# Optimization experiments

Hardware: AMD Instinct MI355X
Metric: run time of the kernel (lower is better)

## Reference

```python
import jax, jax.numpy as jnp
import numpy as np

BATCH = 2048
INPUT_SIZE = 2048
OUTPUT_SIZE = 2048
N_INPUTS = 6            # fan-in per LUT node
K = 1 << N_INPUTS       # 64 table entries per node


def setup_inputs() -> dict:
    key = jax.random.key(0)
    k1, k2, k3 = jax.random.split(key, 3)
    x = jax.random.uniform(k1, (BATCH, INPUT_SIZE), dtype=jnp.float32)
    table = jax.random.normal(k2, (OUTPUT_SIZE, K), dtype=jnp.float32)
    mapping = jax.random.randint(k3, (OUTPUT_SIZE, N_INPUTS), 0, INPUT_SIZE, dtype=jnp.int64)
    return {"x": x, "table": table, "mapping": mapping}


def reference(x, table, mapping):
    # x: (B, I) in [0,1]; table: (O, 2^n) raw logits; mapping: (O, n) int indices
    O, n = mapping.shape
    Kv = 1 << n
    # per-node input gather -> (B, O, n)
    xg = x[:, mapping]
    # binary codes of the 2^n LUT vertices: bits[k, i] = i-th bit of k
    bits = ((jnp.arange(Kv)[:, None] >> jnp.arange(n)[None, :]) & 1).astype(x.dtype)  # (K, n)
    # vertex probabilities prod_i (x_i if bit else 1-x_i), built by a tiny fixed loop over n
    probs = jnp.ones((x.shape[0], O, Kv), dtype=x.dtype)
    for i in range(n):
        xi = xg[:, :, i][:, :, None]                      # (B, O, 1)
        bi = bits[:, i][None, None, :]                    # (1, 1, K)
        probs = probs * (xi * bi + (1.0 - xi) * (1.0 - bi))
    # differentiable LUT lookup: expected table value under vertex distribution
    out = jnp.einsum('bok,ok->bo', probs, jax.nn.sigmoid(table))  # (B, O)
    return out
```

## Files before the change

### kernel.cpp

```cpp
#include <hip/hip_runtime.h>
#include <math.h>

#define B_TOTAL 2048
#define I_TOTAL 2048
#define O_TOTAL 2048
#define KW 64
#define NIN 6
#define BLOCK 256

#define WS_SIGW 0
#define WS_M32  (512 * 1024)
#define WS_XT   (1024 * 1024)
#define WS_OUTT (WS_XT + B_TOTAL * I_TOTAL * 4)

__global__ void prep_kernel(const float* __restrict__ table,
                            const unsigned int* __restrict__ map_raw,
                            float* __restrict__ sigw,
                            int* __restrict__ m32)
{
    int idx = blockIdx.x * blockDim.x + threadIdx.x;
    int k = idx & 63;
    float s = 1.0f / (1.0f + __expf(-table[idx]));
    float v = s;
    if (k >= 32) {
        float s0 = 1.0f / (1.0f + __expf(-table[idx - 32]));
        v = s - s0;
    }
    sigw[idx] = v;

    if (idx < O_TOTAL * NIN) {
        bool is64 = ((map_raw[1] | map_raw[3] | map_raw[5] | map_raw[7]) == 0u);
        m32[idx] = is64 ? (int)map_raw[2 * idx] : (int)map_raw[idx];
    }
}

__global__ __launch_bounds__(256) void transpose_k(const float* __restrict__ src,
                                                   float* __restrict__ dst)
{
    __shared__ float tile[64][65];
    const int t  = threadIdx.x;
    const int r0 = blockIdx.y * 64;
    const int c0 = blockIdx.x * 64;
    const int rr = t >> 4;
    const int cc = (t & 15) << 2;
    #pragma unroll
    for (int p = 0; p < 4; ++p) {
        int r = p * 16 + rr;
        float4 v = *(const float4*)(src + (size_t)(r0 + r) * 2048 + c0 + cc);
        tile[r][cc + 0] = v.x; tile[r][cc + 1] = v.y;
        tile[r][cc + 2] = v.z; tile[r][cc + 3] = v.w;
    }
    __syncthreads();
    #pragma unroll
    for (int p = 0; p < 4; ++p) {
        int r = p * 16 + rr;
        float4 v;
        v.x = tile[cc + 0][r]; v.y = tile[cc + 1][r];
        v.z = tile[cc + 2][r]; v.w = tile[cc + 3][r];
        *(float4*)(dst + (size_t)(c0 + r) * 2048 + r0 + cc) = v;
    }
}

__global__ __launch_bounds__(BLOCK) void lut_main(
    const float* __restrict__ xT,
    const float* __restrict__ sigw,
    const int*   __restrict__ m32,
    float*       __restrict__ outT)
{
    const int wave = threadIdx.x >> 6;
    const int lane = threadIdx.x & 63;
    const int o    = blockIdx.y * 4 + wave;
    const int b0   = blockIdx.x * 512;

    float ww[KW];
    const float* wp = sigw + (size_t)o * KW;
    #pragma unroll
    for (int k = 0; k < KW; ++k) ww[k] = wp[k];

    int m[NIN];
    #pragma unroll
    for (int i = 0; i < NIN; ++i) m[i] = m32[o * NIN + i];

    #pragma unroll
    for (int p = 0; p < 8; ++p) {
        const int b = b0 + p * 64 + lane;
        float xv[NIN];
        #pragma unroll
        for (int i = 0; i < NIN; ++i)
            xv[i] = xT[(size_t)m[i] * B_TOTAL + b];

        float t[32];
        #pragma unroll
        for (int j = 0; j < 32; ++j) t[j] = fmaf(xv[5], ww[j + 32], ww[j]);
        #pragma unroll
        for (int j = 0; j < 16; ++j) t[j] = fmaf(xv[4], t[j + 16] - t[j], t[j]);
        #pragma unroll
        for (int j = 0; j < 8;  ++j) t[j] = fmaf(xv[3], t[j + 8]  - t[j], t[j]);
        #pragma unroll
        for (int j = 0; j < 4;  ++j) t[j] = fmaf(xv[2], t[j + 4]  - t[j], t[j]);
        #pragma unroll
        for (int j = 0; j < 2;  ++j) t[j] = fmaf(xv[1], t[j + 2]  - t[j], t[j]);
        float res = fmaf(xv[0], t[1] - t[0], t[0]);

        outT[(size_t)o * B_TOTAL + b] = res;
    }
}

extern "C" void kernel_launch(void* const* d_in, const int* in_sizes, int n_in,
                              void* d_out, int out_size, void* d_ws, size_t ws_size,
                              hipStream_t stream)
{
    const float*        x       = (const float*)d_in[0];
    const float*        table   = (const float*)d_in[1];
    const unsigned int* map_raw = (const unsigned int*)d_in[2];
    float* out  = (float*)d_out;
    float* sigw = (float*)((char*)d_ws + WS_SIGW);
    int*   m32  = (int*)  ((char*)d_ws + WS_M32);
    float* xT   = (float*)((char*)d_ws + WS_XT);
    float* outT = (float*)((char*)d_ws + WS_OUTT);

    prep_kernel<<<(O_TOTAL * KW) / BLOCK, BLOCK, 0, stream>>>(table, map_raw, sigw, m32);
    transpose_k<<<dim3(32, 32), BLOCK, 0, stream>>>(x, xT);

    lut_main<<<dim3(4, 512), BLOCK, 0, stream>>>(xT, sigw, m32, outT);

    transpose_k<<<dim3(32, 32), BLOCK, 0, stream>>>(outT, out);
}
```

Measured before the change: 95.84 us.

## Fuse prep into input transpose and transpose output in LUT kernel via LDS

Merges the sigmoid/mapping prep kernel into the input transpose kernel, removing one launch. The LUT kernel now computes a 64x64 (output node x batch) tile per block and transposes it through shared memory, writing the final output directly instead of going through a separate output transpose kernel and a temporary buffer. Each wave now loops over 16 nodes, reloading the 64 weights for each node instead of keeping them resident across 512 batch rows, so weight reloads increase.

```diff
diff --git a/kernel.cpp b/kernel.cpp
--- a/kernel.cpp
+++ b/kernel.cpp
@@ -11,31 +11,14 @@
 #define WS_SIGW 0
 #define WS_M32  (512 * 1024)
 #define WS_XT   (1024 * 1024)
-#define WS_OUTT (WS_XT + B_TOTAL * I_TOTAL * 4)
 
-__global__ void prep_kernel(const float* __restrict__ table,
-                            const unsigned int* __restrict__ map_raw,
-                            float* __restrict__ sigw,
-                            int* __restrict__ m32)
-{
-    int idx = blockIdx.x * blockDim.x + threadIdx.x;
-    int k = idx & 63;
-    float s = 1.0f / (1.0f + __expf(-table[idx]));
-    float v = s;
-    if (k >= 32) {
-        float s0 = 1.0f / (1.0f + __expf(-table[idx - 32]));
-        v = s - s0;
-    }
-    sigw[idx] = v;
-
-    if (idx < O_TOTAL * NIN) {
-        bool is64 = ((map_raw[1] | map_raw[3] | map_raw[5] | map_raw[7]) == 0u);
-        m32[idx] = is64 ? (int)map_raw[2 * idx] : (int)map_raw[idx];
-    }
-}
-
-__global__ __launch_bounds__(256) void transpose_k(const float* __restrict__ src,
-                                                   float* __restrict__ dst)
+__global__ __launch_bounds__(BLOCK) void xpose_prep(
+    const float* __restrict__ x,
+    const float* __restrict__ table,
+    const unsigned int* __restrict__ map_raw,
+    float* __restrict__ xT,
+    float* __restrict__ sigw,
+    int* __restrict__ m32)
 {
     __shared__ float tile[64][65];
     const int t  = threadIdx.x;
@@ -46,10 +29,28 @@
     #pragma unroll
     for (int p = 0; p < 4; ++p) {
         int r = p * 16 + rr;
-        float4 v = *(const float4*)(src + (size_t)(r0 + r) * 2048 + c0 + cc);
+        float4 v = *(const float4*)(x + (size_t)(r0 + r) * I_TOTAL + c0 + cc);
         tile[r][cc + 0] = v.x; tile[r][cc + 1] = v.y;
         tile[r][cc + 2] = v.z; tile[r][cc + 3] = v.w;
     }
+
+    const int bid = blockIdx.y * gridDim.x + blockIdx.x;
+    const int gid = bid * BLOCK + t;
+    if (gid < O_TOTAL * KW) {
+        int k = gid & 63;
+        float s = 1.0f / (1.0f + __expf(-table[gid]));
+        float v = s;
+        if (k >= 32) {
+            float s0 = 1.0f / (1.0f + __expf(-table[gid - 32]));
+            v = s - s0;
+        }
+        sigw[gid] = v;
+    }
+    if (gid < O_TOTAL * NIN) {
+        bool is64 = ((map_raw[1] | map_raw[3] | map_raw[5] | map_raw[7]) == 0u);
+        m32[gid] = is64 ? (int)map_raw[2 * gid] : (int)map_raw[gid];
+    }
+
     __syncthreads();
     #pragma unroll
     for (int p = 0; p < 4; ++p) {
@@ -57,7 +58,7 @@
         float4 v;
         v.x = tile[cc + 0][r]; v.y = tile[cc + 1][r];
         v.z = tile[cc + 2][r]; v.w = tile[cc + 3][r];
-        *(float4*)(dst + (size_t)(c0 + r) * 2048 + r0 + cc) = v;
+        *(float4*)(xT + (size_t)(c0 + r) * B_TOTAL + r0 + cc) = v;
     }
 }
 
@@ -65,44 +66,57 @@
     const float* __restrict__ xT,
     const float* __restrict__ sigw,
     const int*   __restrict__ m32,
-    float*       __restrict__ outT)
+    float*       __restrict__ out)
 {
-    const int wave = threadIdx.x >> 6;
-    const int lane = threadIdx.x & 63;
-    const int o    = blockIdx.y * 4 + wave;
-    const int b0   = blockIdx.x * 512;
+    __shared__ float tile[64][65];
+    const int tid  = threadIdx.x;
+    const int lane = tid & 63;
+    const int wv   = __builtin_amdgcn_readfirstlane(tid >> 6);
+    const int o0   = blockIdx.x * 64;
+    const int b    = blockIdx.y * 64 + lane;
 
-    float ww[KW];
-    const float* wp = sigw + (size_t)o * KW;
-    #pragma unroll
-    for (int k = 0; k < KW; ++k) ww[k] = wp[k];
+    #pragma unroll 2
+    for (int j = 0; j < 16; ++j) {
+        const int o = o0 + wv * 16 + j;
+        const float* __restrict__ wp = sigw + (size_t)o * KW;
+        const int*   __restrict__ mp = m32 + o * NIN;
 
-    int m[NIN];
-    #pragma unroll
-    for (int i = 0; i < NIN; ++i) m[i] = m32[o * NIN + i];
+        int m[NIN];
+        #pragma unroll
+        for (int i = 0; i < NIN; ++i) m[i] = mp[i];
 
-    #pragma unroll
-    for (int p = 0; p < 8; ++p) {
-        const int b = b0 + p * 64 + lane;
         float xv[NIN];
         #pragma unroll
         for (int i = 0; i < NIN; ++i)
             xv[i] = xT[(size_t)m[i] * B_TOTAL + b];
 
+        float ww[KW];
+        #pragma unroll
+        for (int k = 0; k < KW; ++k) ww[k] = wp[k];
+
         float t[32];
         #pragma unroll
-        for (int j = 0; j < 32; ++j) t[j] = fmaf(xv[5], ww[j + 32], ww[j]);
+        for (int q = 0; q < 32; ++q) t[q] = fmaf(xv[5], ww[q + 32], ww[q]);
         #pragma unroll
-        for (int j = 0; j < 16; ++j) t[j] = fmaf(xv[4], t[j + 16] - t[j], t[j]);
+        for (int q = 0; q < 16; ++q) t[q] = fmaf(xv[4], t[q + 16] - t[q], t[q]);
         #pragma unroll
-        for (int j = 0; j < 8;  ++j) t[j] = fmaf(xv[3], t[j + 8]  - t[j], t[j]);
+        for (int q = 0; q < 8;  ++q) t[q] = fmaf(xv[3], t[q + 8]  - t[q], t[q]);
         #pragma unroll
-        for (int j = 0; j < 4;  ++j) t[j] = fmaf(xv[2], t[j + 4]  - t[j], t[j]);
+        for (int q = 0; q < 4;  ++q) t[q] = fmaf(xv[2], t[q + 4]  - t[q], t[q]);
         #pragma unroll
-        for (int j = 0; j < 2;  ++j) t[j] = fmaf(xv[1], t[j + 2]  - t[j], t[j]);
+        for (int q = 0; q < 2;  ++q) t[q] = fmaf(xv[1], t[q + 2]  - t[q], t[q]);
         float res = fmaf(xv[0], t[1] - t[0], t[0]);
 
-        outT[(size_t)o * B_TOTAL + b] = res;
+        tile[wv * 16 + j][lane] = res;
+    }
+
+    __syncthreads();
+    #pragma unroll
+    for (int r = 0; r < 16; ++r) {
+        const int e  = r * BLOCK + tid;
+        const int bl = e >> 6;
+        const int ol = e & 63;
+        out[(size_t)(blockIdx.y * 64 + bl) * O_TOTAL + o0 + ol] = tile[ol][bl];
     }
 }
 
@@ -117,12 +131,7 @@
     float* sigw = (float*)((char*)d_ws + WS_SIGW);
     int*   m32  = (int*)  ((char*)d_ws + WS_M32);
     float* xT   = (float*)((char*)d_ws + WS_XT);
-    float* outT = (float*)((char*)d_ws + WS_OUTT);
 
-    prep_kernel<<<(O_TOTAL * KW) / BLOCK, BLOCK, 0, stream>>>(table, map_raw, sigw, m32);
-    transpose_k<<<dim3(32, 32), BLOCK, 0, stream>>>(x, xT);
-
-    lut_main<<<dim3(4, 512), BLOCK, 0, stream>>>(xT, sigw, m32, outT);
-
-    transpose_k<<<dim3(32, 32), BLOCK, 0, stream>>>(outT, out);
+    xpose_prep<<<dim3(32, 32), BLOCK, 0, stream>>>(x, table, map_raw, xT, sigw, m32);
+    lut_main<<<dim3(32, 32), BLOCK, 0, stream>>>(xT, sigw, m32, out);
 }
```

Result: no change. 95.29 us (-0.6%).
